# Kernel optimization log

Measured on AMD Instinct MI355X. Metric: run time of the kernel, lower is better.

The kernel has to match this reference:

```python
import jax, jax.numpy as jnp
import numpy as np

H = 2048          # hidden_size
I_MOE = 1408      # moe_intermediate_size (per expert)
I_SH = 5632       # shared_expert_intermediate_size
E = 8             # num_experts
TOP_K = 2         # num_experts_per_tok
B, S = 1, 2048


def setup_inputs() -> dict:
    key = jax.random.key(0)
    ks = jax.random.split(key, 7)
    sc = 0.02
    return {
        "hidden_states": jax.random.normal(ks[0], (B, S, H), jnp.float32),
        "W_router": jax.random.normal(ks[1], (E, H), jnp.float32) * sc,      # gate.weight
        "W_sgate": jax.random.normal(ks[2], (1, H), jnp.float32) * sc,       # shared_expert_gate.weight
        "Ws_gate_up": jax.random.normal(ks[3], (H, 2 * I_SH), jnp.float32) * sc,  # shared expert merged gate/up
        "Ws_down": jax.random.normal(ks[4], (I_SH, H), jnp.float32) * sc,
        "We_gate_up": jax.random.normal(ks[5], (E, H, 2 * I_MOE), jnp.float32) * sc,  # stacked expert gate/up
        "We_down": jax.random.normal(ks[6], (E, I_MOE, H), jnp.float32) * sc,
    }


def _silu_and_mul(gu, inter):
    # gate_up layout: [..., 2*inter] -> silu(gate) * up, matching SiluAndMul
    return jax.nn.silu(gu[..., :inter]) * gu[..., inter:]


def reference(hidden_states, W_router, W_sgate, Ws_gate_up, Ws_down, We_gate_up, We_down):
    orig_shape = hidden_states.shape
    x = hidden_states.reshape(-1, H)                     # [T, H]
    T = x.shape[0]

    # --- router: softmax in fp32 then top-k (NOT renormalized, as in source) ---
    logits = x @ W_router.T                              # [T, E]
    probs = jax.nn.softmax(logits.astype(jnp.float32), axis=-1)
    rw, sel = jax.lax.top_k(probs, TOP_K)                # [T, K]
    rw = rw.astype(x.dtype)

    # sparse combine matrix [T, E]: routing weight where selected, else 0
    combine = jnp.zeros((T, E), x.dtype).at[jnp.arange(T)[:, None], sel].add(rw)

    # --- shared expert ---
    sh = _silu_and_mul(x @ Ws_gate_up, I_SH) @ Ws_down    # [T, H]
    shared_out = sh * jax.nn.sigmoid(x @ W_sgate.T)       # [T, H]

    # --- experts: dense dispatch (math-identical to gather/MLP/index_add loop) ---
    gu = jnp.einsum('th,ehi->eti', x, We_gate_up)         # [E, T, 2*I_MOE]
    h = _silu_and_mul(gu, I_MOE)                          # [E, T, I_MOE]
    eo = jnp.einsum('eti,eih->eth', h, We_down)           # [E, T, H]
    sparse_out = jnp.einsum('eth,te->th', eo, combine)    # [T, H]

    return (shared_out + sparse_out).reshape(orig_shape)
```

## Files before the change

### kernel.cpp

```cpp
#include <hip/hip_runtime.h>
#include <cstdio>


#define H_DIM 2048
#define IMOE  1408
#define ISH   5632
#define NEXP  8
#define T_TOK 2048
#define TK_TOT (T_TOK * 2)

typedef __attribute__((ext_vector_type(8))) short short8;
typedef __attribute__((ext_vector_type(8))) __bf16 bf16x8;
typedef __attribute__((ext_vector_type(4))) float f32x4;

__device__ __forceinline__ float bf2f(unsigned short u) {
  union { unsigned int i; float f; } v; v.i = ((unsigned int)u) << 16; return v.f;
}
__device__ __forceinline__ unsigned short f2bf(float f) {
  union { float f; unsigned int i; } v; v.f = f;
  unsigned int x = v.i;
  return (unsigned short)((x + 0x7fffu + ((x >> 16) & 1u)) >> 16);
}

__device__ __forceinline__ f32x4 MFMA16(short8 a, short8 b, f32x4 c) {
  return __builtin_amdgcn_mfma_f32_16x16x32_bf16(
      __builtin_bit_cast(bf16x8, a), __builtin_bit_cast(bf16x8, b), c, 0, 0, 0);
}

__device__ __forceinline__ void gload_lds16(const unsigned short* g, unsigned short* l) {
  __builtin_amdgcn_global_load_lds(
      (const __attribute__((address_space(1))) unsigned int*)g,
      (__attribute__((address_space(3))) unsigned int*)l, 16, 0, 0);
}

__device__ __forceinline__ float silu_f(float x) { return x / (1.0f + __expf(-x)); }

#define SBAR()   asm volatile("s_barrier" ::: "memory")
#define VMCNT(n) asm volatile("s_waitcnt vmcnt(" #n ")" ::: "memory")
#define LGKM0()  asm volatile("s_waitcnt lgkmcnt(0)" ::: "memory")


__global__ __launch_bounds__(256)
void transpose_cvt_kernel(const float* __restrict__ src, unsigned short* __restrict__ dst,
                          int R, int C, long sStride, long dStride) {
  src += (long)blockIdx.z * sStride;
  dst += (long)blockIdx.z * dStride;
  __shared__ float tile[32][33];
  int tx = threadIdx.x, ty = threadIdx.y;
  int x = blockIdx.x * 32 + tx;
  int yb = blockIdx.y * 32;
#pragma unroll
  for (int j = 0; j < 4; j++) {
    int y = yb + ty + j * 8;
    tile[ty + j * 8][tx] = src[(long)y * C + x];
  }
  __syncthreads();
  int c = blockIdx.x * 32 + ty;
  int r = yb + tx;
#pragma unroll
  for (int j = 0; j < 4; j++) {
    dst[(long)(c + j * 8) * R + r] = f2bf(tile[tx][ty + j * 8]);
  }
}

__global__ __launch_bounds__(256)
void cvt_x_kernel(const float* __restrict__ x, unsigned short* __restrict__ xb, int total4) {
  int i = blockIdx.x * 256 + threadIdx.x;
  if (i >= total4) return;
  float4 v = ((const float4*)x)[i];
  ushort4 o;
  o.x = f2bf(v.x); o.y = f2bf(v.y); o.z = f2bf(v.z); o.w = f2bf(v.w);
  ((ushort4*)xb)[i] = o;
}


__global__ __launch_bounds__(256)
void router_kernel(const float* __restrict__ x, const float* __restrict__ Wr,
                   const float* __restrict__ Wsg, float* __restrict__ rw,
                   int* __restrict__ sel, float* __restrict__ sgate_sig,
                   int* __restrict__ counts) {
  int t = blockIdx.x;
  const float* xr = x + (long)t * H_DIM;
  float p[9];
#pragma unroll
  for (int e = 0; e < 9; e++) p[e] = 0.0f;
  for (int h = threadIdx.x; h < H_DIM; h += 256) {
    float xv = xr[h];
#pragma unroll
    for (int e = 0; e < 8; e++) p[e] += xv * Wr[e * H_DIM + h];
    p[8] += xv * Wsg[h];
  }
#pragma unroll
  for (int e = 0; e < 9; e++)
    for (int off = 32; off > 0; off >>= 1)
      p[e] += __shfl_down(p[e], off, 64);
  __shared__ float red[4][9];
  int wave = threadIdx.x >> 6, lane = threadIdx.x & 63;
  if (lane == 0) {
#pragma unroll
    for (int e = 0; e < 9; e++) red[wave][e] = p[e];
  }
  __syncthreads();
  if (threadIdx.x == 0) {
    float lg[9];
#pragma unroll
    for (int e = 0; e < 9; e++) lg[e] = red[0][e] + red[1][e] + red[2][e] + red[3][e];
    float m = lg[0];
#pragma unroll
    for (int e = 1; e < 8; e++) m = fmaxf(m, lg[e]);
    float pr[8], s = 0.0f;
#pragma unroll
    for (int e = 0; e < 8; e++) { pr[e] = expf(lg[e] - m); s += pr[e]; }
    float inv = 1.0f / s;
#pragma unroll
    for (int e = 0; e < 8; e++) pr[e] *= inv;
    int i0 = 0;
#pragma unroll
    for (int e = 1; e < 8; e++) if (pr[e] > pr[i0]) i0 = e;
    int i1 = (i0 == 0) ? 1 : 0;
#pragma unroll
    for (int e = 0; e < 8; e++) if (e != i0 && pr[e] > pr[i1]) i1 = e;
    rw[t * 2] = pr[i0]; rw[t * 2 + 1] = pr[i1];
    sel[t * 2] = i0;    sel[t * 2 + 1] = i1;
    sgate_sig[t] = 1.0f / (1.0f + expf(-lg[8]));
    atomicAdd(&counts[i0], 1);
    atomicAdd(&counts[i1], 1);
  }
}

__global__ void scan_kernel(const int* __restrict__ counts, int* __restrict__ offsets) {
  if (threadIdx.x == 0 && blockIdx.x == 0) {
    int s = 0;
    for (int e = 0; e < NEXP; e++) { offsets[e] = s; s += counts[e]; }
    offsets[NEXP] = s;
  }
}

__global__ __launch_bounds__(256)
void scatter_kernel(const int* __restrict__ sel, const int* __restrict__ offsets,
                    int* __restrict__ cursor, int* __restrict__ tok_of_slot,
                    int* __restrict__ slot_of_tok) {
  int t = blockIdx.x * 256 + threadIdx.x;
  if (t >= T_TOK) return;
#pragma unroll
  for (int k = 0; k < 2; k++) {
    int e = sel[t * 2 + k];
    int pos = atomicAdd(&cursor[e], 1);
    int slot = offsets[e] + pos;
    tok_of_slot[slot] = t;
    slot_of_tok[t * 2 + k] = slot;
  }
}

__global__ __launch_bounds__(256)
void gather_kernel(const unsigned short* __restrict__ xbf, const int* __restrict__ tok,
                   unsigned short* __restrict__ xg) {
  int i = blockIdx.x * 256 + threadIdx.x;
  int slot = i >> 8, c8 = i & 255;
  long src = (long)tok[slot] * H_DIM + c8 * 8;
  ulonglong2 v = *(const ulonglong2*)(xbf + src);
  ((ulonglong2*)xg)[i] = v;
}

template <int PHASE>
__global__ __launch_bounds__(512, 2)
void moe_gemm8_kernel(const unsigned short* __restrict__ Ash,
                      const unsigned short* __restrict__ Bsh,
                      const unsigned short* __restrict__ Aex,
                      const unsigned short* __restrict__ Bex,
                      void* __restrict__ Csh, void* __restrict__ Cex,
                      const int* __restrict__ counts,
                      const int* __restrict__ offsets,
                      const float* __restrict__ rowscale) {
  int o = blockIdx.x;
  int b = (o & 7) * (gridDim.x >> 3) + (o >> 3);

  const unsigned short *A, *B;
  char* Cc;
  int N, Kld, NT, row0, col0, rowbase = 0, cnt;
  int epi;
  if constexpr (PHASE == 0) {
    if (b < 352) {
      A = Ash; B = Bsh; Cc = (char*)Csh; epi = 0;
      N = 2 * ISH; Kld = H_DIM; NT = H_DIM / 64;
      row0 = (b & 7) * 256; col0 = (b >> 3) * 256; cnt = T_TOK;
    } else {
      int b2 = b - 352, e = b2 / 88, r2 = b2 % 88;
      cnt = counts[e]; row0 = (r2 & 7) * 256;
      if (row0 >= cnt) return;
      rowbase = offsets[e];
      A = Aex; B = Bex + (long)e * 2 * IMOE * H_DIM; Cc = (char*)Cex; epi = 0;
      N = 2 * IMOE; Kld = H_DIM; NT = H_DIM / 64;
      col0 = (r2 >> 3) * 256;
    }
  } else {
    if (b < 64) {
      A = Ash; B = Bsh; Cc = (char*)Csh; epi = 1;
      N = H_DIM; Kld = ISH; NT = ISH / 64;
      row0 = (b & 7) * 256; col0 = (b >> 3) * 256; cnt = T_TOK;
    } else {
      int b2 = b - 64, e = b2 >> 6, r2 = b2 & 63;
      cnt = counts[e]; row0 = (r2 & 7) * 256;
      if (row0 >= cnt) return;
      rowbase = offsets[e];
      A = Aex; B = Bex + (long)e * H_DIM * IMOE; Cc = (char*)Cex; epi = 2;
      N = H_DIM; Kld = IMOE; NT = IMOE / 64;
      col0 = (r2 >> 3) * 256;
    }
  }

  __shared__ unsigned short lds8[65536];

  int tid = threadIdx.x, wave = tid >> 6, lane = tid & 63;
  int wr = wave >> 2, wc = wave & 3;
  int fr = lane & 15, fg = lane >> 4;

  int cK[2];
  cK[0] = fr * 64 + ((fg ^ (fr & 7)) * 8);
  cK[1] = fr * 64 + (((4 + fg) ^ (fr & 7)) * 8);
  int aBase = wr * 8192;
  int bBase = 32768 + (wc >> 1) * 8192 + (wc & 1) * 4096;

  const unsigned short *pA[2][2], *pB[2][2];
#pragma unroll
  for (int h = 0; h < 2; h++)
#pragma unroll
    for (int s = 0; s < 2; s++) {
      int hr = s * 64 + wave * 8 + (lane >> 3);
      int g = (lane & 7) ^ (hr & 7);
      long ra = row0 + h * 128 + hr;
      if (ra > cnt - 1) ra = cnt - 1;
      ra += rowbase;
      pA[h][s] = A + ra * (long)Kld + g * 8;
      pB[h][s] = B + (long)(col0 + h * 128 + hr) * Kld + g * 8;
    }

#define STG_A(d, h, tile) do { long ko = (long)(tile) * 64; \
    gload_lds16(pA[h][0] + ko, &lds8[(d)*16384 + (h)*8192 + wave*512]); \
    gload_lds16(pA[h][1] + ko, &lds8[(d)*16384 + (h)*8192 + 4096 + wave*512]); } while (0)
#define STG_B(d, h, tile) do { long ko = (long)(tile) * 64; \
    gload_lds16(pB[h][0] + ko, &lds8[32768 + (d)*16384 + (h)*8192 + wave*512]); \
    gload_lds16(pB[h][1] + ko, &lds8[32768 + (d)*16384 + (h)*8192 + 4096 + wave*512]); } while (0)

  short8 aReg[4][2], bReg[4][2];
  f32x4 acc[8][4] = {};

#define LDA(mh, d) do { _Pragma("unroll") for (int mi = 0; mi < 4; mi++) \
    _Pragma("unroll") for (int k = 0; k < 2; k++) \
      aReg[mi][k] = *(const short8*)&lds8[(d)*16384 + aBase + ((mh)*4 + mi)*1024 + cK[k]]; } while (0)
#define LDB(nh, d) do { _Pragma("unroll") for (int ni = 0; ni < 2; ni++) \
    _Pragma("unroll") for (int k = 0; k < 2; k++) \
      bReg[(nh)*2 + ni][k] = *(const short8*)&lds8[(d)*16384 + bBase + ((nh)*2 + ni)*1024 + cK[k]]; } while (0)
#define MM(mh, nh) do { _Pragma("unroll") for (int mi = 0; mi < 4; mi++) \
    _Pragma("unroll") for (int ni = 0; ni < 2; ni++) \
    _Pragma("unroll") for (int k = 0; k < 2; k++) \
      acc[(mh)*4 + mi][(nh)*2 + ni] = \
          MFMA16(aReg[mi][k], bReg[(nh)*2 + ni][k], acc[(mh)*4 + mi][(nh)*2 + ni]); } while (0)
#define PH_MID() do { SBAR(); LGKM0(); __builtin_amdgcn_s_setprio(1); } while (0)
#define PH_END() do { __builtin_amdgcn_s_setprio(0); SBAR(); } while (0)

  STG_B(0, 0, 0); STG_B(0, 1, 0);
  STG_A(0, 0, 0); STG_A(0, 1, 0);
  STG_B(1, 0, 1); STG_B(1, 1, 1);
  VMCNT(4);
  SBAR();

  int NI = NT >> 1;
  for (int i = 0; i < NI; i++) {
    int t1 = 2 * i + 1;
    int t2 = 2 * i + 2; if (t2 > NT - 1) t2 = NT - 1;
    int t3 = 2 * i + 3; if (t3 > NT - 1) t3 = NT - 1;
    LDA(0, 0); LDB(0, 0); STG_A(1, 0, t1);
    PH_MID(); MM(0, 0); PH_END();
    LDB(1, 0); STG_A(1, 1, t1);
    PH_MID(); MM(0, 1); PH_END();
    LDA(1, 0); STG_B(0, 0, t2);
    PH_MID(); MM(1, 0); PH_END();
    STG_B(0, 1, t2);
    PH_MID(); MM(1, 1);
    __builtin_amdgcn_s_setprio(0); VMCNT(4); SBAR();
    LDA(0, 1); LDB(0, 1); STG_A(0, 0, t2);
    PH_MID(); MM(0, 0); PH_END();
    LDB(1, 1); STG_A(0, 1, t2);
    PH_MID(); MM(0, 1); PH_END();
    LDA(1, 1); STG_B(1, 0, t3);
    PH_MID(); MM(1, 0); PH_END();
    STG_B(1, 1, t3);
    PH_MID(); MM(1, 1);
    __builtin_amdgcn_s_setprio(0); VMCNT(4); SBAR();
  }
  VMCNT(0);

  int rowguard = cnt - row0;
#pragma unroll
  for (int m = 0; m < 8; m++) {
    int rl = wr * 128 + m * 16 + fg * 4;
#pragma unroll
    for (int n = 0; n < 4; n++) {
      int cg = col0 + wc * 64 + n * 16 + fr;
      f32x4 v = acc[m][n];
#pragma unroll
      for (int j = 0; j < 4; j++) {
        int r = rl + j;
        if (r < rowguard) {
          long orow = (long)rowbase + row0 + r;
          long ci = orow * (long)N + cg;
          if (epi == 0)      ((unsigned short*)Cc)[ci] = f2bf(v[j]);
          else if (epi == 1) ((float*)Cc)[ci] = v[j] * rowscale[orow];
          else               ((float*)Cc)[ci] = v[j];
        }
      }
    }
  }
#undef STG_A
#undef STG_B
#undef LDA
#undef LDB
#undef MM
#undef PH_MID
#undef PH_END
}


__global__ __launch_bounds__(256)
void silu2_kernel(const unsigned short* __restrict__ gu_sh, unsigned short* __restrict__ h_sh,
                  const unsigned short* __restrict__ gu_e, unsigned short* __restrict__ h_e) {
  int i = blockIdx.x * 256 + threadIdx.x;
  const int nsh = T_TOK * (ISH / 4);
  const unsigned short* g;
  unsigned short* h;
  int I, row, c4;
  if (i < nsh) {
    g = gu_sh; h = h_sh; I = ISH;
    row = i / (ISH / 4); c4 = i - row * (ISH / 4);
  } else {
    int j = i - nsh;
    g = gu_e; h = h_e; I = IMOE;
    row = j / (IMOE / 4); c4 = j - row * (IMOE / 4);
  }
  const unsigned short* gp = g + (long)row * 2 * I + c4 * 4;
  ushort4 gv = *(const ushort4*)gp;
  ushort4 uv = *(const ushort4*)(gp + I);
  ushort4 o2;
  o2.x = f2bf(silu_f(bf2f(gv.x)) * bf2f(uv.x));
  o2.y = f2bf(silu_f(bf2f(gv.y)) * bf2f(uv.y));
  o2.z = f2bf(silu_f(bf2f(gv.z)) * bf2f(uv.z));
  o2.w = f2bf(silu_f(bf2f(gv.w)) * bf2f(uv.w));
  *(ushort4*)(h + (long)row * I + c4 * 4) = o2;
}

__global__ __launch_bounds__(256)
void combine_kernel(float* __restrict__ out, const float* __restrict__ eo,
                    const int* __restrict__ slot_of_tok, const float* __restrict__ rw) {
  int i = blockIdx.x * 256 + threadIdx.x;
  const int h4n = H_DIM / 4;
  if (i >= T_TOK * h4n) return;
  int t = i / h4n;
  int h4 = i - t * h4n;
  int s0 = slot_of_tok[t * 2], s1 = slot_of_tok[t * 2 + 1];
  float w0 = rw[t * 2], w1 = rw[t * 2 + 1];
  float4 o = ((float4*)out)[i];
  float4 a = ((const float4*)eo)[(long)s0 * h4n + h4];
  float4 b = ((const float4*)eo)[(long)s1 * h4n + h4];
  o.x += w0 * a.x + w1 * b.x;
  o.y += w0 * a.y + w1 * b.y;
  o.z += w0 * a.z + w1 * b.z;
  o.w += w0 * a.w + w1 * b.w;
  ((float4*)out)[i] = o;
}


extern "C" void kernel_launch(void* const* d_in, const int* in_sizes, int n_in,
                              void* d_out, int out_size, void* d_ws, size_t ws_size,
                              hipStream_t stream) {
  (void)in_sizes; (void)n_in; (void)out_size;
  const float* x    = (const float*)d_in[0];
  const float* Wr   = (const float*)d_in[1];
  const float* Wsg  = (const float*)d_in[2];
  const float* Wsgu = (const float*)d_in[3];
  const float* Wsd  = (const float*)d_in[4];
  const float* Wegu = (const float*)d_in[5];
  const float* Wed  = (const float*)d_in[6];
  float* out = (float*)d_out;

  char* ws = (char*)d_ws;
  size_t off = 0;
  auto alloc = [&](size_t b) { size_t o = off; off += (b + 255) & ~(size_t)255; return o; };

  size_t o_xbf   = alloc((size_t)T_TOK * H_DIM * 2);
  size_t o_WsguT = alloc((size_t)2 * ISH * H_DIM * 2);
  size_t o_WsdT  = alloc((size_t)H_DIM * ISH * 2);
  size_t o_WeguT = alloc((size_t)NEXP * 2 * IMOE * H_DIM * 2);
  size_t o_WedT  = alloc((size_t)NEXP * H_DIM * IMOE * 2);
  size_t o_gush  = alloc((size_t)T_TOK * 2 * ISH * 2);
  size_t o_hsh   = alloc((size_t)T_TOK * ISH * 2);
  size_t o_gue   = alloc((size_t)TK_TOT * 2 * IMOE * 2);
  size_t o_xg    = alloc((size_t)TK_TOT * H_DIM * 2);
  size_t o_ints  = alloc(256);
  size_t o_rw    = alloc((size_t)TK_TOT * 4);
  size_t o_sel   = alloc((size_t)TK_TOT * 4);
  size_t o_sg    = alloc((size_t)T_TOK * 4);
  size_t o_tok   = alloc((size_t)TK_TOT * 4);
  size_t o_s2t   = alloc((size_t)TK_TOT * 4);

  if (off > ws_size) {
    fprintf(stderr, "[moe kernel] workspace too small: need %zu have %zu\n", off, ws_size);
    return;
  }

  unsigned short* xbf   = (unsigned short*)(ws + o_xbf);
  unsigned short* WsguT = (unsigned short*)(ws + o_WsguT);
  unsigned short* WsdT  = (unsigned short*)(ws + o_WsdT);
  unsigned short* WeguT = (unsigned short*)(ws + o_WeguT);
  unsigned short* WedT  = (unsigned short*)(ws + o_WedT);
  unsigned short* gu_sh = (unsigned short*)(ws + o_gush);
  unsigned short* h_sh  = (unsigned short*)(ws + o_hsh);
  unsigned short* gu_e  = (unsigned short*)(ws + o_gue);
  unsigned short* xg    = (unsigned short*)(ws + o_xg);
  unsigned short* h_e   = (unsigned short*)(ws + o_WeguT);
  float* eo             = (float*)(ws + o_WsguT);

  int* counts  = (int*)(ws + o_ints);
  int* cursor  = counts + 8;
  int* offsets = counts + 16;
  float* rw    = (float*)(ws + o_rw);
  int* sel     = (int*)(ws + o_sel);
  float* sgate = (float*)(ws + o_sg);
  int* tok     = (int*)(ws + o_tok);
  int* s2t     = (int*)(ws + o_s2t);

  dim3 tb(32, 8, 1);

  hipMemsetAsync(counts, 0, 64, stream);

  transpose_cvt_kernel<<<dim3(2 * ISH / 32, H_DIM / 32, 1), tb, 0, stream>>>(
      Wsgu, WsguT, H_DIM, 2 * ISH, 0, 0);
  transpose_cvt_kernel<<<dim3(H_DIM / 32, ISH / 32, 1), tb, 0, stream>>>(
      Wsd, WsdT, ISH, H_DIM, 0, 0);
  transpose_cvt_kernel<<<dim3(2 * IMOE / 32, H_DIM / 32, NEXP), tb, 0, stream>>>(
      Wegu, WeguT, H_DIM, 2 * IMOE, (long)H_DIM * 2 * IMOE, (long)2 * IMOE * H_DIM);
  transpose_cvt_kernel<<<dim3(H_DIM / 32, IMOE / 32, NEXP), tb, 0, stream>>>(
      Wed, WedT, IMOE, H_DIM, (long)IMOE * H_DIM, (long)H_DIM * IMOE);

  cvt_x_kernel<<<(T_TOK * H_DIM / 4) / 256, 256, 0, stream>>>(x, xbf, T_TOK * H_DIM / 4);

  router_kernel<<<T_TOK, 256, 0, stream>>>(x, Wr, Wsg, rw, sel, sgate, counts);
  scan_kernel<<<1, 64, 0, stream>>>(counts, offsets);
  scatter_kernel<<<(T_TOK + 255) / 256, 256, 0, stream>>>(sel, offsets, cursor, tok, s2t);
  gather_kernel<<<TK_TOT, 256, 0, stream>>>(xbf, tok, xg);

  moe_gemm8_kernel<0><<<1056, 512, 0, stream>>>(
      xbf, WsguT, xg, WeguT, gu_sh, gu_e, counts, offsets, nullptr);

  {
    int total = T_TOK * (ISH / 4) + TK_TOT * (IMOE / 4);
    silu2_kernel<<<total / 256, 256, 0, stream>>>(gu_sh, h_sh, gu_e, h_e);
  }

  moe_gemm8_kernel<1><<<576, 512, 0, stream>>>(
      h_sh, WsdT, h_e, WedT, out, eo, counts, offsets, sgate);

  combine_kernel<<<(T_TOK * H_DIM / 4) / 256, 256, 0, stream>>>(out, eo, s2t, rw);
}
```

Measured before the change: 856.7 us.

## Split-K the shared down-projection across four slices with atomic accumulation

The shared-expert down GEMM (K=5632) is split into four K slices, raising its block count from 64 to 256. Each slice adds its partial result into the output with float atomics, so the output buffer is now zeroed with a memset beforehand. LDS fragment reads are also changed to inline ds_read_b128 with precomputed byte addresses, plus a sched_barrier. The aim is better CU occupancy in phase 1, at the cost of atomic traffic, an extra memset and non-deterministic summation order.

```diff
diff --git a/kernel.cpp b/kernel.cpp
--- a/kernel.cpp
+++ b/kernel.cpp
@@ -38,6 +38,7 @@
 #define SBAR()   asm volatile("s_barrier" ::: "memory")
 #define VMCNT(n) asm volatile("s_waitcnt vmcnt(" #n ")" ::: "memory")
 #define LGKM0()  asm volatile("s_waitcnt lgkmcnt(0)" ::: "memory")
+#define DSR(dst, a) asm volatile("ds_read_b128 %0, %1" : "=v"(dst) : "v"(a))
 
 
 __global__ __launch_bounds__(256)
@@ -177,7 +178,7 @@
 
   const unsigned short *A, *B;
   char* Cc;
-  int N, Kld, NT, row0, col0, rowbase = 0, cnt;
+  int N, Kld, NT, row0, col0, rowbase = 0, cnt, k0 = 0;
   int epi;
   if constexpr (PHASE == 0) {
     if (b < 352) {
@@ -194,12 +195,13 @@
       col0 = (r2 >> 3) * 256;
     }
   } else {
-    if (b < 64) {
+    if (b < 256) {
       A = Ash; B = Bsh; Cc = (char*)Csh; epi = 1;
-      N = H_DIM; Kld = ISH; NT = ISH / 64;
-      row0 = (b & 7) * 256; col0 = (b >> 3) * 256; cnt = T_TOK;
+      N = H_DIM; Kld = ISH; NT = (ISH / 4) / 64;
+      row0 = (b & 7) * 256; col0 = ((b >> 3) & 7) * 256; cnt = T_TOK;
+      k0 = (b >> 6) * (ISH / 4);
     } else {
-      int b2 = b - 64, e = b2 >> 6, r2 = b2 & 63;
+      int b2 = b - 256, e = b2 >> 6, r2 = b2 & 63;
       cnt = counts[e]; row0 = (r2 & 7) * 256;
       if (row0 >= cnt) return;
       rowbase = offsets[e];
@@ -215,11 +217,13 @@
   int wr = wave >> 2, wc = wave & 3;
   int fr = lane & 15, fg = lane >> 4;
 
-  int cK[2];
-  cK[0] = fr * 64 + ((fg ^ (fr & 7)) * 8);
-  cK[1] = fr * 64 + (((4 + fg) ^ (fr & 7)) * 8);
-  int aBase = wr * 8192;
-  int bBase = 32768 + (wc >> 1) * 8192 + (wc & 1) * 4096;
+  unsigned ldsbase = (unsigned)(size_t)lds8;
+  unsigned sK0 = (unsigned)(((fg) ^ (fr & 7)) * 16);
+  unsigned sK1 = (unsigned)(((4 + fg) ^ (fr & 7)) * 16);
+  unsigned aBk0 = ldsbase + (unsigned)(wr * 16384 + fr * 128) + sK0;
+  unsigned aBk1 = ldsbase + (unsigned)(wr * 16384 + fr * 128) + sK1;
+  unsigned bBk0 = ldsbase + 65536u + (unsigned)((wc >> 1) * 16384 + (wc & 1) * 8192 + fr * 128) + sK0;
+  unsigned bBk1 = ldsbase + 65536u + (unsigned)((wc >> 1) * 16384 + (wc & 1) * 8192 + fr * 128) + sK1;
 
   const unsigned short *pA[2][2], *pB[2][2];
 #pragma unroll
@@ -231,8 +235,8 @@
       long ra = row0 + h * 128 + hr;
       if (ra > cnt - 1) ra = cnt - 1;
       ra += rowbase;
-      pA[h][s] = A + ra * (long)Kld + g * 8;
-      pB[h][s] = B + (long)(col0 + h * 128 + hr) * Kld + g * 8;
+      pA[h][s] = A + ra * (long)Kld + k0 + g * 8;
+      pB[h][s] = B + (long)(col0 + h * 128 + hr) * Kld + k0 + g * 8;
     }
 
 #define STG_A(d, h, tile) do { long ko = (long)(tile) * 64; \
@@ -245,18 +249,19 @@
   short8 aReg[4][2], bReg[4][2];
   f32x4 acc[8][4] = {};
 
-#define LDA(mh, d) do { _Pragma("unroll") for (int mi = 0; mi < 4; mi++) \
-    _Pragma("unroll") for (int k = 0; k < 2; k++) \
-      aReg[mi][k] = *(const short8*)&lds8[(d)*16384 + aBase + ((mh)*4 + mi)*1024 + cK[k]]; } while (0)
-#define LDB(nh, d) do { _Pragma("unroll") for (int ni = 0; ni < 2; ni++) \
-    _Pragma("unroll") for (int k = 0; k < 2; k++) \
-      bReg[(nh)*2 + ni][k] = *(const short8*)&lds8[(d)*16384 + bBase + ((nh)*2 + ni)*1024 + cK[k]]; } while (0)
+#define LDA(mh, d) do { _Pragma("unroll") for (int mi = 0; mi < 4; mi++) { \
+      DSR(aReg[mi][0], aBk0 + (unsigned)((d)*32768 + ((mh)*4 + mi)*2048)); \
+      DSR(aReg[mi][1], aBk1 + (unsigned)((d)*32768 + ((mh)*4 + mi)*2048)); } } while (0)
+#define LDB(nh, d) do { _Pragma("unroll") for (int ni = 0; ni < 2; ni++) { \
+      DSR(bReg[(nh)*2 + ni][0], bBk0 + (unsigned)((d)*32768 + ((nh)*2 + ni)*2048)); \
+      DSR(bReg[(nh)*2 + ni][1], bBk1 + (unsigned)((d)*32768 + ((nh)*2 + ni)*2048)); } } while (0)
 #define MM(mh, nh) do { _Pragma("unroll") for (int mi = 0; mi < 4; mi++) \
     _Pragma("unroll") for (int ni = 0; ni < 2; ni++) \
     _Pragma("unroll") for (int k = 0; k < 2; k++) \
       acc[(mh)*4 + mi][(nh)*2 + ni] = \
           MFMA16(aReg[mi][k], bReg[(nh)*2 + ni][k], acc[(mh)*4 + mi][(nh)*2 + ni]); } while (0)
-#define PH_MID() do { SBAR(); LGKM0(); __builtin_amdgcn_s_setprio(1); } while (0)
+#define PH_MID() do { SBAR(); LGKM0(); __builtin_amdgcn_sched_barrier(0); \
+                      __builtin_amdgcn_s_setprio(1); } while (0)
 #define PH_END() do { __builtin_amdgcn_s_setprio(0); SBAR(); } while (0)
 
   STG_B(0, 0, 0); STG_B(0, 1, 0);
@@ -306,7 +311,7 @@
           long orow = (long)rowbase + row0 + r;
           long ci = orow * (long)N + cg;
           if (epi == 0)      ((unsigned short*)Cc)[ci] = f2bf(v[j]);
-          else if (epi == 1) ((float*)Cc)[ci] = v[j] * rowscale[orow];
+          else if (epi == 1) unsafeAtomicAdd(&((float*)Cc)[ci], v[j] * rowscale[orow]);
           else               ((float*)Cc)[ci] = v[j];
         }
       }
@@ -432,6 +437,7 @@
   dim3 tb(32, 8, 1);
 
   hipMemsetAsync(counts, 0, 64, stream);
+  hipMemsetAsync(out, 0, (size_t)T_TOK * H_DIM * 4, stream);
 
   transpose_cvt_kernel<<<dim3(2 * ISH / 32, H_DIM / 32, 1), tb, 0, stream>>>(
       Wsgu, WsguT, H_DIM, 2 * ISH, 0, 0);
@@ -457,7 +463,7 @@
     silu2_kernel<<<total / 256, 256, 0, stream>>>(gu_sh, h_sh, gu_e, h_e);
   }
 
-  moe_gemm8_kernel<1><<<576, 512, 0, stream>>>(
+  moe_gemm8_kernel<1><<<768, 512, 0, stream>>>(
       h_sh, WsdT, h_e, WedT, out, eo, counts, offsets, sgate);
 
   combine_kernel<<<(T_TOK * H_DIM / 4) / 256, 256, 0, stream>>>(out, eo, s2t, rw);
```

After: 881.1 us. 1.03x slower.
